# Kernel tuning notes

Hardware: AMD Instinct MI355X
Metric: run time of the kernel (lower is better)

Reference implementation:

```python
import jax, jax.numpy as jnp
import numpy as np

N, K, D, V = 20000, 16, 256, 64  # nodes, neighbors, embed_dim, edge vocab


def setup_inputs() -> dict:
    key = jax.random.key(0)
    ks = jax.random.split(key, 16)
    s = 1.0 / np.sqrt(2 * D)  # Linear(512 -> 256) init scale
    return {
        "node_reps": jax.random.normal(ks[0], (1, N, D), jnp.float32),
        "in_indices": jax.random.randint(ks[1], (1, N, K), 0, N, jnp.int32),
        "in_edges": jax.random.randint(ks[2], (1, N, K), 0, V, jnp.int32),
        "in_mask": jax.random.uniform(ks[3], (1, N, K), jnp.float32),
        "out_indices": jax.random.randint(ks[4], (1, N, K), 0, N, jnp.int32),
        "out_edges": jax.random.randint(ks[5], (1, N, K), 0, V, jnp.int32),
        "out_mask": jax.random.uniform(ks[6], (1, N, K), jnp.float32),
        "edge_emb_1": jax.random.normal(ks[7], (V, D), jnp.float32),
        "W_1": jax.random.uniform(ks[8], (2 * D, D), jnp.float32, -s, s),
        "b_1": jnp.zeros((D,), jnp.float32),
        "edge_emb_2": jax.random.normal(ks[9], (V, D), jnp.float32),
        "W_2": jax.random.uniform(ks[10], (2 * D, D), jnp.float32, -s, s),
        "b_2": jnp.zeros((D,), jnp.float32),
        "edge_emb_3": jax.random.normal(ks[11], (V, D), jnp.float32),
        "W_3": jax.random.uniform(ks[12], (2 * D, D), jnp.float32, -s, s),
        "b_3": jnp.zeros((D,), jnp.float32),
    }


def gcn_layer(node_reps, in_idx, in_edg, in_msk, out_idx, out_edg, out_msk,
              edge_emb, W, b):
    # node_reps: [1, N, D]; dropout is identity in eval mode.
    nodes = node_reps[0]  # [N, D]; batch_size == 1 as in the original repo

    def agg(idx, edg, msk):
        nbr = nodes[idx]          # gather: [1, N, K, D]
        erep = edge_emb[edg]      # embedding lookup: [1, N, K, D]
        reps = jnp.concatenate([nbr, erep], axis=3) * msk[..., None]
        return reps.sum(axis=2)   # masked sum over neighbors: [1, N, 2D]

    in_reps = agg(in_idx, in_edg, in_msk)
    out_reps = agg(out_idx, out_edg, out_msk)
    in_nodes = in_reps[0] @ W + b    # [N, D]
    out_nodes = out_reps[0] @ W + b  # [N, D]
    return node_reps + out_nodes + in_nodes  # broadcast -> [1, N, D]


def reference(node_reps, in_indices, in_edges, in_mask,
              out_indices, out_edges, out_mask,
              edge_emb_1, W_1, b_1, edge_emb_2, W_2, b_2, edge_emb_3, W_3, b_3):
    nbrs = (in_indices, in_edges, in_mask, out_indices, out_edges, out_mask)
    hidden = gcn_layer(node_reps, *nbrs, edge_emb_1, W_1, b_1)  # gc1
    mu = gcn_layer(hidden, *nbrs, edge_emb_2, W_2, b_2)          # gc2
    logvar = gcn_layer(hidden, *nbrs, edge_emb_3, W_3, b_3)      # gc3

    mu_t = jnp.tanh(mu[0])        # [N, D]
    lv_t = jnp.tanh(logvar[0])    # [N, D]
    n_nodes = mu_t.shape[0]
    kld = (-0.5 / n_nodes) * jnp.mean(
        jnp.sum(1.0 + 2.0 * lv_t - mu_t ** 2 - jnp.exp(lv_t) ** 2, axis=1))
    return hidden, kld
```

## Files before the change

kernel.cpp:

```cpp
#include <hip/hip_runtime.h>
#include <math.h>

#define NN 20000
#define KK 16
#define DD 256
#define VV 64
#define NT1 16
#define SAS 336
#define SAS8 336

typedef __attribute__((ext_vector_type(8))) __bf16 bf16x8;
typedef __attribute__((ext_vector_type(4))) float floatx4;
typedef __attribute__((ext_vector_type(2))) float floatx2;
typedef __attribute__((ext_vector_type(8))) unsigned short ushort8;
typedef __attribute__((ext_vector_type(4))) unsigned int uint4v;

__device__ __forceinline__ float4 ld4(const float* p) { return *reinterpret_cast<const float4*>(p); }

__device__ __forceinline__ unsigned short f2bf(float f) {
    union { float f; unsigned u; } v; v.f = f;
    unsigned r = v.u + 0x7FFFu + ((v.u >> 16) & 1u);
    return (unsigned short)(r >> 16);
}
__device__ __forceinline__ float bf2f(unsigned short u) {
    union { unsigned u; float f; } v; v.u = ((unsigned)u) << 16;
    return v.f;
}
__device__ __forceinline__ unsigned char f2q(float f) {
    return (unsigned char)(__builtin_amdgcn_cvt_pk_fp8_f32(f, 0.f, 0u, false) & 0xFFu);
}
__device__ __forceinline__ float q2f(unsigned char q) {
    floatx2 r = __builtin_amdgcn_cvt_pk_f32_fp8((unsigned)q, false);
    return r.x;
}
__device__ __forceinline__ float ftanh(float v) {
    float e = __expf(2.f * v);
    return 1.f - 2.f * __builtin_amdgcn_rcpf(e + 1.f);
}

__global__ __launch_bounds__(256) void ewhist(
    const int* __restrict__ ie, const float* __restrict__ im,
    const int* __restrict__ oe, const float* __restrict__ om,
    const float* __restrict__ x,
    const float* __restrict__ e1, const float* __restrict__ W1,
    const float* __restrict__ e2, const float* __restrict__ W2,
    const float* __restrict__ e3, const float* __restrict__ W3,
    float* __restrict__ EW, unsigned short* __restrict__ Hc,
    unsigned short* __restrict__ xh, float* __restrict__ kld) {
    int blk = blockIdx.x, tid = threadIdx.x;
    if (blk < 192) {
        int layer = blk >> 6, v = blk & 63, d = tid;
        const float* emb = layer == 0 ? e1 : (layer == 1 ? e2 : e3);
        const float* W   = layer == 0 ? W1 : (layer == 1 ? W2 : W3);
        float acc = 0.f;
        #pragma unroll 8
        for (int j = 0; j < 256; ++j)
            acc += emb[v * DD + j] * W[(size_t)(256 + j) * DD + d];
        EW[(size_t)layer * VV * DD + v * DD + d] = acc;
    } else {
        int pb = blk - 192;
        int w = tid >> 6, lane = tid & 63;
        int n = pb * 4 + w;
        int e = 0; float m = 0.f;
        if (lane < 16)      { e = ie[n * KK + lane];      m = im[n * KK + lane]; }
        else if (lane < 32) { e = oe[n * KK + lane - 16]; m = om[n * KK + lane - 16]; }
        float h = 0.f;
        #pragma unroll
        for (int j = 0; j < 32; ++j) {
            int ev = __shfl(e, j);
            float mv = __shfl(m, j);
            if (ev == lane) h += mv;
        }
        Hc[(size_t)n * 64 + lane] = f2bf(h);
        size_t base = (size_t)pb * 1024 + tid * 4;
        float4 v = ld4(x + base);
        ushort4 o; o.x = f2bf(v.x); o.y = f2bf(v.y); o.z = f2bf(v.z); o.w = f2bf(v.w);
        *reinterpret_cast<ushort4*>(xh + base) = o;
        if (pb == 0 && tid == 0) *kld = 0.f;
    }
}

__global__ __launch_bounds__(256) void packU(
    const float* __restrict__ W1, const float* __restrict__ W2, const float* __restrict__ W3,
    const float* __restrict__ EW,
    unsigned short* __restrict__ U1, unsigned short* __restrict__ U23) {
    int blk = blockIdx.x, tid = threadIdx.x;
    int u1path = blk < 40;
    int NT = u1path ? 16 : 32;
    int g = (u1path ? blk : blk - 40) * 256 + tid;
    int lane = g & 63, ntk = g >> 6;
    int nt = ntk % NT, kt = ntk / NT;
    if (kt >= 10) return;
    int n = nt * 16 + (lane & 15);
    int kbase = kt * 32 + (lane >> 4) * 8;
    const float* W; const float* EWl;
    if (u1path)       { W = W1; EWl = EW; }
    else if (n < 256) { W = W2; EWl = EW + VV * DD; }
    else              { W = W3; EWl = EW + 2 * VV * DD; n -= 256; }
    unsigned short o8[8];
    #pragma unroll
    for (int j = 0; j < 8; ++j) {
        int k = kbase + j;
        float v = (k < 256) ? W[(size_t)k * DD + n] : EWl[(size_t)(k - 256) * DD + n];
        o8[j] = f2bf(v);
    }
    unsigned short* U = u1path ? U1 : U23;
    *reinterpret_cast<uint4v*>(&U[(size_t)g * 8]) = *reinterpret_cast<uint4v*>(o8);
}

__global__ __launch_bounds__(256) void fmm1(const unsigned short* __restrict__ xh, const unsigned short* __restrict__ Hc,
                                            const int* __restrict__ ii, const float* __restrict__ im,
                                            const int* __restrict__ oi, const float* __restrict__ om,
                                            const unsigned short* __restrict__ U, const float* __restrict__ b,
                                            float* __restrict__ out, unsigned char* __restrict__ h8) {
    __shared__ unsigned short sA[16 * SAS];
    __shared__ int sidx[16][32];
    __shared__ float smsk[16][32];
    int n0 = blockIdx.x * 16;
    int tid = threadIdx.x;
    for (int q = tid; q < 512; q += 256) {
        int r = q >> 5, j = q & 31;
        int n = n0 + r;
        sidx[r][j] = (j < 16) ? ii[n * KK + j] : oi[n * KK + j - 16];
        smsk[r][j] = (j < 16) ? im[n * KK + j] : om[n * KK + j - 16];
    }
    if (tid < 128) {
        int r = tid >> 3, k8 = tid & 7;
        *reinterpret_cast<uint4v*>(&sA[r * SAS + 256 + k8 * 8]) =
            *reinterpret_cast<const uint4v*>(&Hc[(size_t)(n0 + r) * 64 + k8 * 8]);
    }
    __syncthreads();
    int lane = tid & 63, w = tid >> 6;
    int half = lane >> 5, c = (lane & 31) * 8;
    #pragma unroll
    for (int rr = 0; rr < 4; ++rr) {
        int row = w * 4 + rr;
        float acc[8] = {0.f, 0.f, 0.f, 0.f, 0.f, 0.f, 0.f, 0.f};
        #pragma unroll
        for (int j = 0; j < 16; ++j) {
            int j2 = j * 2 + half;
            int idx = sidx[row][j2];
            float m = smsk[row][j2];
            ushort8 u = *reinterpret_cast<const ushort8*>(xh + (size_t)idx * DD + c);
            #pragma unroll
            for (int z = 0; z < 8; ++z) acc[z] += m * bf2f(u[z]);
        }
        #pragma unroll
        for (int z = 0; z < 8; ++z) acc[z] += __shfl_xor(acc[z], 32);
        if (half == 0) {
            unsigned short o8[8];
            #pragma unroll
            for (int z = 0; z < 8; ++z) o8[z] = f2bf(acc[z]);
            *reinterpret_cast<uint4v*>(&sA[row * SAS + c]) = *reinterpret_cast<uint4v*>(o8);
        }
    }
    __syncthreads();
    int lr = lane & 15, quad = lane >> 4;
    float xp[4][4], bb[4];
    #pragma unroll
    for (int t = 0; t < 4; ++t) {
        int col = (w * 4 + t) * 16 + lr;
        bb[t] = 2.f * b[col];
        #pragma unroll
        for (int r = 0; r < 4; ++r)
            xp[t][r] = bf2f(xh[(size_t)(n0 + quad * 4 + r) * DD + col]);
    }
    floatx4 z = {0.f, 0.f, 0.f, 0.f};
    floatx4 acc[4] = {z, z, z, z};
    for (int kt = 0; kt < 10; ++kt) {
        bf16x8 a = *reinterpret_cast<const bf16x8*>(&sA[lr * SAS + kt * 32 + quad * 8]);
        #pragma unroll
        for (int t = 0; t < 4; ++t) {
            bf16x8 bf = *reinterpret_cast<const bf16x8*>(&U[(size_t)((kt * NT1 + w * 4 + t) * 64 + lane) * 8]);
            acc[t] = __builtin_amdgcn_mfma_f32_16x16x32_bf16(a, bf, acc[t], 0, 0, 0);
        }
    }
    #pragma unroll
    for (int t = 0; t < 4; ++t) {
        int col = (w * 4 + t) * 16 + lr;
        #pragma unroll
        for (int r = 0; r < 4; ++r) {
            size_t o = (size_t)(n0 + quad * 4 + r) * DD + col;
            float v = xp[t][r] + bb[t] + acc[t][r];
            out[o] = v;
            h8[o] = f2q(v);
        }
    }
}

__global__ __launch_bounds__(256) void fmm23(const unsigned char* __restrict__ h8, const unsigned short* __restrict__ Hc,
                                             const int* __restrict__ ii, const float* __restrict__ im,
                                             const int* __restrict__ oi, const float* __restrict__ om,
                                             const unsigned short* __restrict__ U, const float* __restrict__ b2,
                                             const float* __restrict__ b3, float* __restrict__ kld) {
    __shared__ unsigned short sA[16 * SAS];
    __shared__ int sidx[16][32];
    __shared__ float smsk[16][32];
    __shared__ float red[4];
    int n0 = blockIdx.x * 16;
    int tid = threadIdx.x;
    for (int q = tid; q < 512; q += 256) {
        int r = q >> 5, j = q & 31;
        int n = n0 + r;
        sidx[r][j] = (j < 16) ? ii[n * KK + j] : oi[n * KK + j - 16];
        smsk[r][j] = (j < 16) ? im[n * KK + j] : om[n * KK + j - 16];
    }
    if (tid < 128) {
        int r = tid >> 3, k8 = tid & 7;
        *reinterpret_cast<uint4v*>(&sA[r * SAS + 256 + k8 * 8]) =
            *reinterpret_cast<const uint4v*>(&Hc[(size_t)(n0 + r) * 64 + k8 * 8]);
    }
    __syncthreads();
    int lane = tid & 63, w = tid >> 6;
    int g = lane >> 4, cl = lane & 15;
    #pragma unroll
    for (int rr = 0; rr < 4; ++rr) {
        int row = w * 4 + rr;
        float acc[16];
        #pragma unroll
        for (int z = 0; z < 16; ++z) acc[z] = 0.f;
        #pragma unroll
        for (int j = 0; j < 8; ++j) {
            int r = g * 8 + j;
            int idx = sidx[row][r];
            float m = smsk[row][r];
            uint4v u = *reinterpret_cast<const uint4v*>(h8 + (size_t)idx * DD + cl * 16);
            #pragma unroll
            for (int d = 0; d < 4; ++d) {
                floatx2 f01 = __builtin_amdgcn_cvt_pk_f32_fp8(u[d], false);
                floatx2 f23 = __builtin_amdgcn_cvt_pk_f32_fp8(u[d], true);
                acc[d * 4 + 0] += m * f01.x; acc[d * 4 + 1] += m * f01.y;
                acc[d * 4 + 2] += m * f23.x; acc[d * 4 + 3] += m * f23.y;
            }
        }
        #pragma unroll
        for (int z = 0; z < 16; ++z) {
            acc[z] += __shfl_xor(acc[z], 16);
            acc[z] += __shfl_xor(acc[z], 32);
        }
        if (g == 0) {
            unsigned short o16[16];
            #pragma unroll
            for (int z = 0; z < 16; ++z) o16[z] = f2bf(acc[z]);
            uint4v* dst = reinterpret_cast<uint4v*>(&sA[row * SAS + cl * 16]);
            dst[0] = reinterpret_cast<uint4v*>(o16)[0];
            dst[1] = reinterpret_cast<uint4v*>(o16)[1];
        }
    }
    __syncthreads();
    int lr = lane & 15, quad = lane >> 4;
    float hp[4][4], bm[4], bl[4];
    #pragma unroll
    for (int t = 0; t < 4; ++t) {
        int col = (w * 4 + t) * 16 + lr;
        bm[t] = 2.f * b2[col];
        bl[t] = 2.f * b3[col];
        #pragma unroll
        for (int r = 0; r < 4; ++r)
            hp[t][r] = q2f(h8[(size_t)(n0 + quad * 4 + r) * DD + col]);
    }
    floatx4 z = {0.f, 0.f, 0.f, 0.f};
    floatx4 am[4] = {z, z, z, z};
    floatx4 al[4] = {z, z, z, z};
    for (int kt = 0; kt < 10; ++kt) {
        bf16x8 a = *reinterpret_cast<const bf16x8*>(&sA[lr * SAS + kt * 32 + quad * 8]);
        #pragma unroll
        for (int t = 0; t < 4; ++t) {
            int nt = w * 4 + t;
            bf16x8 bmu = *reinterpret_cast<const bf16x8*>(&U[(size_t)((kt * 32 + nt) * 64 + lane) * 8]);
            bf16x8 blv = *reinterpret_cast<const bf16x8*>(&U[(size_t)((kt * 32 + 16 + nt) * 64 + lane) * 8]);
            am[t] = __builtin_amdgcn_mfma_f32_16x16x32_bf16(a, bmu, am[t], 0, 0, 0);
            al[t] = __builtin_amdgcn_mfma_f32_16x16x32_bf16(a, blv, al[t], 0, 0, 0);
        }
    }
    float kacc = 0.f;
    #pragma unroll
    for (int t = 0; t < 4; ++t) {
        #pragma unroll
        for (int r = 0; r < 4; ++r) {
            float h = hp[t][r];
            float tm = ftanh(h + bm[t] + am[t][r]);
            float tl = ftanh(h + bl[t] + al[t][r]);
            kacc += (1.f - tm * tm) + (2.f * tl - __expf(2.f * tl));
        }
    }
    #pragma unroll
    for (int off = 32; off > 0; off >>= 1) kacc += __shfl_xor(kacc, off);
    if (lane == 0) red[w] = kacc;
    __syncthreads();
    if (tid == 0)
        atomicAdd(kld, (red[0] + red[1] + red[2] + red[3]) * (-0.5f / ((float)NN * (float)NN)));
}

extern "C" void kernel_launch(void* const* d_in, const int* in_sizes, int n_in,
                              void* d_out, int out_size, void* d_ws, size_t ws_size,
                              hipStream_t stream) {
    const float* x  = (const float*)d_in[0];
    const int*   ii = (const int*)d_in[1];
    const int*   ie = (const int*)d_in[2];
    const float* im = (const float*)d_in[3];
    const int*   oi = (const int*)d_in[4];
    const int*   oe = (const int*)d_in[5];
    const float* om = (const float*)d_in[6];
    const float* e1 = (const float*)d_in[7];
    const float* W1 = (const float*)d_in[8];
    const float* b1 = (const float*)d_in[9];
    const float* e2 = (const float*)d_in[10];
    const float* W2 = (const float*)d_in[11];
    const float* b2 = (const float*)d_in[12];
    const float* e3 = (const float*)d_in[13];
    const float* W3 = (const float*)d_in[14];
    const float* b3 = (const float*)d_in[15];
    float* out = (float*)d_out;
    float* kld = out + (size_t)NN * DD;

    char* ws = (char*)d_ws;
    float*          EW  = (float*)(ws);
    unsigned short* U1  = (unsigned short*)(ws + 196608);
    unsigned short* U23 = (unsigned short*)(ws + 360448);
    unsigned short* Hc  = (unsigned short*)(ws + 688128);
    unsigned short* xh  = (unsigned short*)(ws + 3248128);
    unsigned char*  h8  = (unsigned char*)(ws + 13488128);

    ewhist<<<192 + NN / 4, 256, 0, stream>>>(ie, im, oe, om, x, e1, W1, e2, W2, e3, W3,
                                             EW, Hc, xh, kld);
    packU <<<120, 256, 0, stream>>>(W1, W2, W3, EW, U1, U23);
    fmm1  <<<NN / 16, 256, 0, stream>>>(xh, Hc, ii, im, oi, om, U1, b1, out, h8);
    fmm23 <<<NN / 16, 256, 0, stream>>>(h8, Hc, ii, im, oi, om, U23, b2, b3, kld);
}
```

Measured before the change: 192.2 us.

## Fuse weight packing into prep kernel and batch gather loads in aggregation

The separate packU launch is removed. Edge-embedding products are written directly in packed bf16 MFMA layout by the ewhist blocks, and the W rows are packed by extra blocks of the same kernel, dropping one launch and the fp32 EW round trip. In fmm1 all 16 neighbor row loads are issued before accumulation. In fmm23 two rows are processed together, with 16 loads in flight, to raise memory-level parallelism. This costs more registers, which may reduce occupancy.

```diff
diff --git a/kernel.cpp b/kernel.cpp
--- a/kernel.cpp
+++ b/kernel.cpp
@@ -7,7 +7,6 @@
 #define VV 64
 #define NT1 16
 #define SAS 336
-#define SAS8 336
 
 typedef __attribute__((ext_vector_type(8))) __bf16 bf16x8;
 typedef __attribute__((ext_vector_type(4))) float floatx4;
@@ -45,8 +44,9 @@
     const float* __restrict__ e1, const float* __restrict__ W1,
     const float* __restrict__ e2, const float* __restrict__ W2,
     const float* __restrict__ e3, const float* __restrict__ W3,
-    float* __restrict__ EW, unsigned short* __restrict__ Hc,
-    unsigned short* __restrict__ xh, float* __restrict__ kld) {
+    unsigned short* __restrict__ U1, unsigned short* __restrict__ U23,
+    unsigned short* __restrict__ Hc, unsigned short* __restrict__ xh,
+    float* __restrict__ kld) {
     int blk = blockIdx.x, tid = threadIdx.x;
     if (blk < 192) {
         int layer = blk >> 6, v = blk & 63, d = tid;
@@ -56,9 +56,36 @@
         #pragma unroll 8
         for (int j = 0; j < 256; ++j)
             acc += emb[v * DD + j] * W[(size_t)(256 + j) * DD + d];
-        EW[(size_t)layer * VV * DD + v * DD + d] = acc;
+        int kt = 8 + (v >> 5), quadp = (v & 31) >> 3, j = v & 7;
+        if (layer == 0) {
+            int g = (kt * 16 + (d >> 4)) * 64 + quadp * 16 + (d & 15);
+            U1[(size_t)g * 8 + j] = f2bf(acc);
+        } else {
+            int n = (layer == 2) ? 256 + d : d;
+            int g = (kt * 32 + (n >> 4)) * 64 + quadp * 16 + (n & 15);
+            U23[(size_t)g * 8 + j] = f2bf(acc);
+        }
+    } else if (blk < 288) {
+        int blkp = blk - 192;
+        int u1path = blkp < 32;
+        int NT = u1path ? 16 : 32;
+        int g = (u1path ? blkp : blkp - 32) * 256 + tid;
+        int lane = g & 63, ntk = g >> 6;
+        int nt = ntk % NT, kt = ntk / NT;
+        int n = nt * 16 + (lane & 15);
+        int kbase = kt * 32 + (lane >> 4) * 8;
+        const float* W;
+        if (u1path)       { W = W1; }
+        else if (n < 256) { W = W2; }
+        else              { W = W3; n -= 256; }
+        unsigned short o8[8];
+        #pragma unroll
+        for (int j = 0; j < 8; ++j)
+            o8[j] = f2bf(W[(size_t)(kbase + j) * DD + n]);
+        unsigned short* U = u1path ? U1 : U23;
+        *reinterpret_cast<uint4v*>(&U[(size_t)g * 8]) = *reinterpret_cast<uint4v*>(o8);
     } else {
-        int pb = blk - 192;
+        int pb = blk - 288;
         int w = tid >> 6, lane = tid & 63;
         int n = pb * 4 + w;
         int e = 0; float m = 0.f;
@@ -78,34 +105,6 @@
         *reinterpret_cast<ushort4*>(xh + base) = o;
         if (pb == 0 && tid == 0) *kld = 0.f;
     }
-}
-
-__global__ __launch_bounds__(256) void packU(
-    const float* __restrict__ W1, const float* __restrict__ W2, const float* __restrict__ W3,
-    const float* __restrict__ EW,
-    unsigned short* __restrict__ U1, unsigned short* __restrict__ U23) {
-    int blk = blockIdx.x, tid = threadIdx.x;
-    int u1path = blk < 40;
-    int NT = u1path ? 16 : 32;
-    int g = (u1path ? blk : blk - 40) * 256 + tid;
-    int lane = g & 63, ntk = g >> 6;
-    int nt = ntk % NT, kt = ntk / NT;
-    if (kt >= 10) return;
-    int n = nt * 16 + (lane & 15);
-    int kbase = kt * 32 + (lane >> 4) * 8;
-    const float* W; const float* EWl;
-    if (u1path)       { W = W1; EWl = EW; }
-    else if (n < 256) { W = W2; EWl = EW + VV * DD; }
-    else              { W = W3; EWl = EW + 2 * VV * DD; n -= 256; }
-    unsigned short o8[8];
-    #pragma unroll
-    for (int j = 0; j < 8; ++j) {
-        int k = kbase + j;
-        float v = (k < 256) ? W[(size_t)k * DD + n] : EWl[(size_t)(k - 256) * DD + n];
-        o8[j] = f2bf(v);
-    }
-    unsigned short* U = u1path ? U1 : U23;
-    *reinterpret_cast<uint4v*>(&U[(size_t)g * 8]) = *reinterpret_cast<uint4v*>(o8);
 }
 
 __global__ __launch_bounds__(256) void fmm1(const unsigned short* __restrict__ xh, const unsigned short* __restrict__ Hc,
@@ -135,15 +134,16 @@
     #pragma unroll
     for (int rr = 0; rr < 4; ++rr) {
         int row = w * 4 + rr;
+        ushort8 u[16];
+        #pragma unroll
+        for (int j = 0; j < 16; ++j)
+            u[j] = *reinterpret_cast<const ushort8*>(xh + (size_t)sidx[row][j * 2 + half] * DD + c);
         float acc[8] = {0.f, 0.f, 0.f, 0.f, 0.f, 0.f, 0.f, 0.f};
         #pragma unroll
         for (int j = 0; j < 16; ++j) {
-            int j2 = j * 2 + half;
-            int idx = sidx[row][j2];
-            float m = smsk[row][j2];
-            ushort8 u = *reinterpret_cast<const ushort8*>(xh + (size_t)idx * DD + c);
+            float m = smsk[row][j * 2 + half];
             #pragma unroll
-            for (int z = 0; z < 8; ++z) acc[z] += m * bf2f(u[z]);
+            for (int z = 0; z < 8; ++z) acc[z] += m * bf2f(u[j][z]);
         }
         #pragma unroll
         for (int z = 0; z < 8; ++z) acc[z] += __shfl_xor(acc[z], 32);
@@ -214,37 +214,50 @@
     int lane = tid & 63, w = tid >> 6;
     int g = lane >> 4, cl = lane & 15;
     #pragma unroll
-    for (int rr = 0; rr < 4; ++rr) {
-        int row = w * 4 + rr;
-        float acc[16];
-        #pragma unroll
-        for (int z = 0; z < 16; ++z) acc[z] = 0.f;
+    for (int pr = 0; pr < 2; ++pr) {
+        int rowA = w * 4 + pr * 2, rowB = rowA + 1;
+        uint4v ua[8], ub[8];
         #pragma unroll
         for (int j = 0; j < 8; ++j) {
-            int r = g * 8 + j;
-            int idx = sidx[row][r];
-            float m = smsk[row][r];
-            uint4v u = *reinterpret_cast<const uint4v*>(h8 + (size_t)idx * DD + cl * 16);
+            ua[j] = *reinterpret_cast<const uint4v*>(h8 + (size_t)sidx[rowA][g * 8 + j] * DD + cl * 16);
+            ub[j] = *reinterpret_cast<const uint4v*>(h8 + (size_t)sidx[rowB][g * 8 + j] * DD + cl * 16);
+        }
+        float accA[16], accB[16];
+        #pragma unroll
+        for (int z = 0; z < 16; ++z) { accA[z] = 0.f; accB[z] = 0.f; }
+        #pragma unroll
+        for (int j = 0; j < 8; ++j) {
+            float ma = smsk[rowA][g * 8 + j];
+            float mb = smsk[rowB][g * 8 + j];
             #pragma unroll
             for (int d = 0; d < 4; ++d) {
-                floatx2 f01 = __builtin_amdgcn_cvt_pk_f32_fp8(u[d], false);
-                floatx2 f23 = __builtin_amdgcn_cvt_pk_f32_fp8(u[d], true);
-                acc[d * 4 + 0] += m * f01.x; acc[d * 4 + 1] += m * f01.y;
-                acc[d * 4 + 2] += m * f23.x; acc[d * 4 + 3] += m * f23.y;
+                floatx2 a01 = __builtin_amdgcn_cvt_pk_f32_fp8(ua[j][d], false);
+                floatx2 a23 = __builtin_amdgcn_cvt_pk_f32_fp8(ua[j][d], true);
+                accA[d * 4 + 0] += ma * a01.x; accA[d * 4 + 1] += ma * a01.y;
+                accA[d * 4 + 2] += ma * a23.x; accA[d * 4 + 3] += ma * a23.y;
+                floatx2 b01 = __builtin_amdgcn_cvt_pk_f32_fp8(ub[j][d], false);
+                floatx2 b23 = __builtin_amdgcn_cvt_pk_f32_fp8(ub[j][d], true);
+                accB[d * 4 + 0] += mb * b01.x; accB[d * 4 + 1] += mb * b01.y;
+                accB[d * 4 + 2] += mb * b23.x; accB[d * 4 + 3] += mb * b23.y;
             }
         }
         #pragma unroll
         for (int z = 0; z < 16; ++z) {
-            acc[z] += __shfl_xor(acc[z], 16);
-            acc[z] += __shfl_xor(acc[z], 32);
+            accA[z] += __shfl_xor(accA[z], 16);
+            accA[z] += __shfl_xor(accA[z], 32);
+            accB[z] += __shfl_xor(accB[z], 16);
+            accB[z] += __shfl_xor(accB[z], 32);
         }
         if (g == 0) {
-            unsigned short o16[16];
+            unsigned short oA[16], oB[16];
             #pragma unroll
-            for (int z = 0; z < 16; ++z) o16[z] = f2bf(acc[z]);
-            uint4v* dst = reinterpret_cast<uint4v*>(&sA[row * SAS + cl * 16]);
-            dst[0] = reinterpret_cast<uint4v*>(o16)[0];
-            dst[1] = reinterpret_cast<uint4v*>(o16)[1];
+            for (int z = 0; z < 16; ++z) { oA[z] = f2bf(accA[z]); oB[z] = f2bf(accB[z]); }
+            uint4v* dA = reinterpret_cast<uint4v*>(&sA[rowA * SAS + cl * 16]);
+            dA[0] = reinterpret_cast<uint4v*>(oA)[0];
+            dA[1] = reinterpret_cast<uint4v*>(oA)[1];
+            uint4v* dB = reinterpret_cast<uint4v*>(&sA[rowB * SAS + cl * 16]);
+            dB[0] = reinterpret_cast<uint4v*>(oB)[0];
+            dB[1] = reinterpret_cast<uint4v*>(oB)[1];
         }
     }
     __syncthreads();
@@ -315,16 +328,14 @@
     float* kld = out + (size_t)NN * DD;
 
     char* ws = (char*)d_ws;
-    float*          EW  = (float*)(ws);
-    unsigned short* U1  = (unsigned short*)(ws + 196608);
-    unsigned short* U23 = (unsigned short*)(ws + 360448);
-    unsigned short* Hc  = (unsigned short*)(ws + 688128);
-    unsigned short* xh  = (unsigned short*)(ws + 3248128);
-    unsigned char*  h8  = (unsigned char*)(ws + 13488128);
-
-    ewhist<<<192 + NN / 4, 256, 0, stream>>>(ie, im, oe, om, x, e1, W1, e2, W2, e3, W3,
-                                             EW, Hc, xh, kld);
-    packU <<<120, 256, 0, stream>>>(W1, W2, W3, EW, U1, U23);
+    unsigned short* U1  = (unsigned short*)(ws);
+    unsigned short* U23 = (unsigned short*)(ws + 163840);
+    unsigned short* Hc  = (unsigned short*)(ws + 491520);
+    unsigned short* xh  = (unsigned short*)(ws + 3051520);
+    unsigned char*  h8  = (unsigned char*)(ws + 13291520);
+
+    ewhist<<<288 + NN / 4, 256, 0, stream>>>(ie, im, oe, om, x, e1, W1, e2, W2, e3, W3,
+                                             U1, U23, Hc, xh, kld);
     fmm1  <<<NN / 16, 256, 0, stream>>>(xh, Hc, ii, im, oi, om, U1, b1, out, h8);
     fmm23 <<<NN / 16, 256, 0, stream>>>(h8, Hc, ii, im, oi, om, U23, b2, b3, kld);
 }
```

New measurement: 192.6 us. About the same (+0.2%).
